# Performance work log

Hardware: AMD Instinct MI355X
Metric: run time of the kernel (lower is better)

The kernel has to match this reference:

```python
import jax, jax.numpy as jnp
import numpy as np

# SOM hyperparameters (match init_kwargs)
M, N_GRID = 32, 32
D = 512
BATCH = 8192
ALPHA = 0.5          # learning_rate
NUM_EPOCH_BP = 5     # hard-coded in call(): self.backprop(self.count, 5)
ITER = 0             # first call: count == 0
RADIUS_FACTOR = 1.1
GAUSSIAN_STD = 0.08
SIGMA = max(M, N_GRID) * RADIUS_FACTOR  # 35.2


def setup_inputs() -> dict:
    key = jax.random.key(0)
    k1, k2 = jax.random.split(key)
    x = jax.random.normal(k1, (BATCH, D), dtype=jnp.float32)
    som_map = jax.random.uniform(k2, (M * N_GRID, D), dtype=jnp.float32)  # RandomUniform(0,1)
    ii, jj = np.meshgrid(np.arange(M), np.arange(N_GRID), indexing='ij')
    locs = jnp.asarray(np.stack([ii.ravel(), jj.ravel()], axis=1), dtype=jnp.int32)  # [N,2]
    return {"x": x, "som_map": som_map, "locs": locs}


def reference(x, som_map, locs):
    # --- feedforward: BMU search ---
    # squared_distance[b,n] = ||x[b] - map[n]||^2, computed without the [B,N,D] blowup
    x2 = jnp.sum(x * x, axis=1, keepdims=True)                 # [B,1]
    m2 = jnp.sum(som_map * som_map, axis=1)[None, :]           # [1,N]
    sqd = x2 + m2 - 2.0 * (x @ som_map.T)                      # [B,N]
    bmu_indices = jnp.argmin(sqd, axis=1)                      # [B]
    bmu_locs = locs[bmu_indices]                               # [B,2] int

    # --- backprop (iter=0, num_epoch=5) ---
    decay = ITER * (ALPHA - 1.0) / (NUM_EPOCH_BP - 1.0)
    radius = SIGMA - decay
    alpha = ALPHA - decay

    # bmu_distance_squares[b,n] = ||locs[n] - bmu_locs[b]||^2 (grid coords)
    diff = locs[None, :, :] - bmu_locs[:, None, :]             # [B,N,2] small (int)
    bmu_d2 = jnp.sum(diff * diff, axis=2).astype(jnp.float32)  # [B,N]
    impact = jnp.exp(-bmu_d2 / (2.0 * (radius * GAUSSIAN_STD) ** 2))  # [B,N]
    lr = impact * alpha                                        # [B,N]

    # weight_update[n,d] = sum_b lr[b,n] * (x[b,d] - map[n,d])
    # = einsum('bn,bd->nd') - map * sum_b lr   (avoids the [B,N,D] intermediate)
    weight_update = jnp.einsum('bn,bd->nd', lr, x) - som_map * jnp.sum(lr, axis=0)[:, None]
    return som_map + weight_update
```

## Files before the change

### kernel.cpp

```cpp
#include <hip/hip_runtime.h>
#include <stdint.h>

#define D 512
#define KTOT 512
#define BATCH 8192
#define NMAP 1024
#define GRID_W 32
#define ALPHA 0.5f
#define C2 15.859712f

typedef __attribute__((ext_vector_type(4))) float f32x4;
typedef __attribute__((ext_vector_type(8))) _Float16 f16x8;
typedef __attribute__((ext_vector_type(8))) unsigned short u16x8;

static __device__ __forceinline__ unsigned short f2h(float f) {
    union { _Float16 h; unsigned short u; } cv;
    cv.h = (_Float16)f;
    return cv.u;
}

__global__ __launch_bounds__(256) void k_prep(const float* __restrict__ x,
                                              const float* __restrict__ map,
                                              unsigned short* __restrict__ As,
                                              unsigned short* __restrict__ Bs,
                                              float* __restrict__ m2,
                                              unsigned long long* __restrict__ packed) {
    int bid = blockIdx.x;
    if (bid < BATCH * (D / 8) / 256) {
        int g = bid * 256 + threadIdx.x;
        if (g < BATCH) packed[g] = 0xFFFFFFFFFFFFFFFFull;
        int b = g >> 6;
        int k8 = (g & 63) << 3;
        const float* xp = x + (size_t)b * D + k8;
        float4 v0 = *(const float4*)xp;
        float4 v1 = *(const float4*)(xp + 4);
        float vv[8] = {v0.x, v0.y, v0.z, v0.w, v1.x, v1.y, v1.z, v1.w};
        u16x8 hi;
        #pragma unroll
        for (int j = 0; j < 8; j++) hi[j] = f2h(vv[j]);
        *(u16x8*)(As + (size_t)b * KTOT + k8) = hi;
    } else {
        int mb = bid - BATCH * (D / 8) / 256;
        int n = mb * 4 + (threadIdx.x >> 6);
        int lane = threadIdx.x & 63;
        const float* mp = map + (size_t)n * D + lane * 8;
        float4 v0 = *(const float4*)mp;
        float4 v1 = *(const float4*)(mp + 4);
        float vv[8] = {v0.x, v0.y, v0.z, v0.w, v1.x, v1.y, v1.z, v1.w};
        u16x8 hi;
        float s = 0.f;
        #pragma unroll
        for (int j = 0; j < 8; j++) {
            s += vv[j] * vv[j];
            hi[j] = f2h(vv[j]);
        }
        *(u16x8*)(Bs + (size_t)n * KTOT + lane * 8) = hi;
        #pragma unroll
        for (int off = 32; off > 0; off >>= 1) s += __shfl_down(s, off);
        if (lane == 0) m2[n] = s;
    }
}

#define BM 128
#define BN 64
#define BK 64

__global__ __launch_bounds__(256) void k_bmu(const unsigned short* __restrict__ As,
                                             const unsigned short* __restrict__ Bs,
                                             const float* __restrict__ m2,
                                             unsigned long long* __restrict__ packed) {
    __shared__ unsigned short Al[BM * BK];
    __shared__ unsigned short Bl[BN * BK];
    const int xcd = blockIdx.x & 7;
    const int j = blockIdx.x >> 3;
    const int b0 = (xcd * 8 + (j & 7)) * BM;
    const int n0 = (j >> 3) * BN;
    const int t = threadIdx.x;
    const int w = t >> 6, l = t & 63;
    const int wm = w >> 1, wn = w & 1;

    f32x4 acc[4][2];
    #pragma unroll
    for (int i = 0; i < 4; i++)
        #pragma unroll
        for (int jj = 0; jj < 2; jj++) acc[i][jj] = (f32x4)(0.f);

    const int srow = l >> 3;
    const int sslot = (l & 7) ^ (l >> 3);
    const unsigned short* agp0 = As + (size_t)(b0 + w * 32 + srow) * KTOT + sslot * 8;
    const unsigned short* bgp0 = Bs + (size_t)(n0 + w * 16 + srow) * KTOT + sslot * 8;

    for (int kt = 0; kt < KTOT; kt += BK) {
        #pragma unroll
        for (int i = 0; i < 4; i++) {
            __builtin_amdgcn_global_load_lds(
                (const __attribute__((address_space(1))) void*)(agp0 + (size_t)i * 8 * KTOT + kt),
                (__attribute__((address_space(3))) void*)(Al + w * 2048 + i * 512), 16, 0, 0);
        }
        #pragma unroll
        for (int i = 0; i < 2; i++) {
            __builtin_amdgcn_global_load_lds(
                (const __attribute__((address_space(1))) void*)(bgp0 + (size_t)i * 8 * KTOT + kt),
                (__attribute__((address_space(3))) void*)(Bl + w * 1024 + i * 512), 16, 0, 0);
        }
        __syncthreads();

        #pragma unroll
        for (int kk = 0; kk < 2; kk++) {
            f16x8 af[4], bfr[2];
            #pragma unroll
            for (int mi = 0; mi < 4; mi++) {
                int r = wm * 64 + mi * 16 + (l & 15);
                int slot = kk * 4 + (l >> 4);
                af[mi] = *(const f16x8*)&Al[r * 64 + ((slot ^ (r & 7)) << 3)];
            }
            #pragma unroll
            for (int nj = 0; nj < 2; nj++) {
                int r = wn * 32 + nj * 16 + (l & 15);
                int slot = kk * 4 + (l >> 4);
                bfr[nj] = *(const f16x8*)&Bl[r * 64 + ((slot ^ (r & 7)) << 3)];
            }
            #pragma unroll
            for (int mi = 0; mi < 4; mi++)
                #pragma unroll
                for (int nj = 0; nj < 2; nj++)
                    acc[mi][nj] = __builtin_amdgcn_mfma_f32_16x16x32_f16(
                        af[mi], bfr[nj], acc[mi][nj], 0, 0, 0);
        }
        __syncthreads();
    }

    float m2v[2];
    #pragma unroll
    for (int nj = 0; nj < 2; nj++)
        m2v[nj] = m2[n0 + wn * 32 + nj * 16 + (l & 15)];

    #pragma unroll
    for (int mi = 0; mi < 4; mi++) {
        #pragma unroll
        for (int reg = 0; reg < 4; reg++) {
            float best = m2v[0] - 2.0f * acc[mi][0][reg];
            int bi = n0 + wn * 32 + (l & 15);
            {
                float v = m2v[1] - 2.0f * acc[mi][1][reg];
                int n = n0 + wn * 32 + 16 + (l & 15);
                if (v < best) { best = v; bi = n; }
            }
            #pragma unroll
            for (int msk = 1; msk <= 8; msk <<= 1) {
                float ov = __shfl_xor(best, msk);
                int oi = __shfl_xor(bi, msk);
                if (ov < best || (ov == best && oi < bi)) { best = ov; bi = oi; }
            }
            if ((l & 15) == 0) {
                unsigned int fb = __float_as_uint(best);
                fb = (fb & 0x80000000u) ? ~fb : (fb | 0x80000000u);
                unsigned long long key =
                    ((unsigned long long)fb << 32) | (unsigned int)bi;
                int row = b0 + wm * 64 + mi * 16 + (l >> 4) * 4 + reg;
                atomicMin(&packed[row], key);
            }
        }
    }
}

__global__ __launch_bounds__(256) void k_scatter(const float* __restrict__ x,
                                                 const unsigned long long* __restrict__ packed,
                                                 float* __restrict__ S,
                                                 int* __restrict__ cnt) {
    __shared__ int list[BATCH];
    __shared__ int cnts[256];
    __shared__ int offs[256];
    int g = blockIdx.x;
    int t = threadIdx.x;
    int b0 = t * (BATCH / 256);

    int mybmu[BATCH / 256];
    int c = 0;
    #pragma unroll
    for (int i = 0; i < BATCH / 256; i++) {
        mybmu[i] = (int)(packed[b0 + i] & 0xFFFFFFFFull);
        c += (mybmu[i] == g) ? 1 : 0;
    }
    cnts[t] = c;
    offs[t] = c;
    __syncthreads();
    #pragma unroll
    for (int s = 1; s < 256; s <<= 1) {
        int v = (t >= s) ? offs[t - s] : 0;
        __syncthreads();
        offs[t] += v;
        __syncthreads();
    }
    int off = offs[t] - cnts[t];
    #pragma unroll
    for (int i = 0; i < BATCH / 256; i++) {
        if (mybmu[i] == g) list[off++] = b0 + i;
    }
    __syncthreads();
    int len = offs[255];

    float a0 = 0.f, a1 = 0.f, c0 = 0.f, c1 = 0.f;
    int i = 0;
    for (; i + 2 <= len; i += 2) {
        const float* xr0 = x + (size_t)list[i] * D;
        const float* xr1 = x + (size_t)list[i + 1] * D;
        a0 += xr0[t]; a1 += xr0[t + 256];
        c0 += xr1[t]; c1 += xr1[t + 256];
    }
    if (i < len) {
        const float* xr = x + (size_t)list[i] * D;
        a0 += xr[t]; a1 += xr[t + 256];
    }
    S[(size_t)g * D + t] = a0 + c0;
    S[(size_t)g * D + t + 256] = a1 + c1;
    if (t == 0) cnt[g] = len;
}

__global__ __launch_bounds__(256) void k_conv1(const float* __restrict__ S,
                                               float* __restrict__ V,
                                               const int* __restrict__ cnt,
                                               float* __restrict__ sum_lr) {
    __shared__ float tbl[GRID_W];
    __shared__ float vc[GRID_W][GRID_W];
    int gi = blockIdx.x;
    int d = blockIdx.y * 256 + threadIdx.x;
    if (threadIdx.x < GRID_W)
        tbl[threadIdx.x] = __expf(-(float)(threadIdx.x * threadIdx.x) / C2);
    __syncthreads();
    float acc[GRID_W];
    #pragma unroll
    for (int nj = 0; nj < GRID_W; nj++) acc[nj] = 0.f;
    for (int gj = 0; gj < GRID_W; gj++) {
        float s = S[(size_t)(gi * GRID_W + gj) * D + d];
        #pragma unroll
        for (int nj = 0; nj < GRID_W; nj++) {
            int dd = nj - gj; dd = dd < 0 ? -dd : dd;
            acc[nj] += tbl[dd] * s;
        }
    }
    #pragma unroll
    for (int nj = 0; nj < GRID_W; nj++)
        V[(size_t)(gi * GRID_W + nj) * D + d] = acc[nj];

    if (blockIdx.x == 0 && blockIdx.y == 0) {
        int t = threadIdx.x;
        #pragma unroll
        for (int j = 0; j < 4; j++) {
            int idx = t * 4 + j;
            int a = idx >> 5, b = idx & 31;
            float s = 0.f;
            for (int gj = 0; gj < GRID_W; gj++) {
                int dd = gj - b; dd = dd < 0 ? -dd : dd;
                s += tbl[dd] * (float)cnt[a * GRID_W + gj];
            }
            vc[a][b] = s;
        }
        __syncthreads();
        #pragma unroll
        for (int j = 0; j < 4; j++) {
            int idx = t * 4 + j;
            int a = idx >> 5, b = idx & 31;
            float s2 = 0.f;
            for (int gg = 0; gg < GRID_W; gg++) {
                int dd = gg - a; dd = dd < 0 ? -dd : dd;
                s2 += tbl[dd] * vc[gg][b];
            }
            sum_lr[idx] = ALPHA * s2;
        }
    }
}

__global__ __launch_bounds__(256) void k_conv2(const float* __restrict__ V,
                                               const float* __restrict__ map,
                                               const float* __restrict__ sum_lr,
                                               float* __restrict__ out) {
    __shared__ float tbl[GRID_W];
    int nj = blockIdx.x;
    int d = blockIdx.y * 256 + threadIdx.x;
    if (threadIdx.x < GRID_W)
        tbl[threadIdx.x] = __expf(-(float)(threadIdx.x * threadIdx.x) / C2);
    __syncthreads();
    float acc[GRID_W];
    #pragma unroll
    for (int ni = 0; ni < GRID_W; ni++) acc[ni] = 0.f;
    for (int gi = 0; gi < GRID_W; gi++) {
        float v = V[(size_t)(gi * GRID_W + nj) * D + d];
        #pragma unroll
        for (int ni = 0; ni < GRID_W; ni++) {
            int dd = ni - gi; dd = dd < 0 ? -dd : dd;
            acc[ni] += tbl[dd] * v;
        }
    }
    #pragma unroll
    for (int ni = 0; ni < GRID_W; ni++) {
        int n = ni * GRID_W + nj;
        out[(size_t)n * D + d] =
            map[(size_t)n * D + d] * (1.0f - sum_lr[n]) + ALPHA * acc[ni];
    }
}

extern "C" void kernel_launch(void* const* d_in, const int* in_sizes, int n_in,
                              void* d_out, int out_size, void* d_ws, size_t ws_size,
                              hipStream_t stream) {
    (void)in_sizes; (void)n_in; (void)out_size; (void)ws_size;
    const float* x = (const float*)d_in[0];
    const float* map = (const float*)d_in[1];
    float* out = (float*)d_out;

    char* ws = (char*)d_ws;
    unsigned long long* packed = (unsigned long long*)(ws);
    float* m2 = (float*)(ws + 65536);
    int* cnt = (int*)(ws + 69632);
    float* sum_lr = (float*)(ws + 73728);
    float* S = (float*)(ws + 77824);
    float* V = (float*)(ws + 2174976);
    unsigned short* As = (unsigned short*)(ws + 4272128);
    unsigned short* Bs = (unsigned short*)(ws + 12660736);

    k_prep<<<BATCH * (D / 8) / 256 + NMAP / 4, 256, 0, stream>>>(x, map, As, Bs, m2, packed);
    k_bmu<<<(BATCH / BM) * (NMAP / BN), 256, 0, stream>>>(As, Bs, m2, packed);
    k_scatter<<<NMAP, 256, 0, stream>>>(x, packed, S, cnt);
    k_conv1<<<dim3(GRID_W, D / 256), 256, 0, stream>>>(S, V, cnt, sum_lr);
    k_conv2<<<dim3(GRID_W, D / 256), 256, 0, stream>>>(V, map, sum_lr, out);
}
```

Before: 83.38 us.

## Double-buffer LDS tiles in BMU GEMM to overlap global loads with MFMA

The BMU distance GEMM now keeps two LDS buffers for the A and B tiles. The next K-tile is issued with global_load_lds while MFMAs run on the current tile, and one barrier per iteration is dropped. The aim is to hide global-to-LDS latency behind compute. In exchange, LDS use doubles (to 48KB per block), which may lower occupancy. The barrier at the end of the loop has to cover completion of the asynchronous loads.

```diff
diff --git a/kernel.cpp b/kernel.cpp
--- a/kernel.cpp
+++ b/kernel.cpp
@@ -69,8 +69,8 @@
                                              const unsigned short* __restrict__ Bs,
                                              const float* __restrict__ m2,
                                              unsigned long long* __restrict__ packed) {
-    __shared__ unsigned short Al[BM * BK];
-    __shared__ unsigned short Bl[BN * BK];
+    __shared__ unsigned short Al[2][BM * BK];
+    __shared__ unsigned short Bl[2][BN * BK];
     const int xcd = blockIdx.x & 7;
     const int j = blockIdx.x >> 3;
     const int b0 = (xcd * 8 + (j & 7)) * BM;
@@ -90,21 +90,27 @@
     const unsigned short* agp0 = As + (size_t)(b0 + w * 32 + srow) * KTOT + sslot * 8;
     const unsigned short* bgp0 = Bs + (size_t)(n0 + w * 16 + srow) * KTOT + sslot * 8;
 
-    for (int kt = 0; kt < KTOT; kt += BK) {
-        #pragma unroll
-        for (int i = 0; i < 4; i++) {
-            __builtin_amdgcn_global_load_lds(
-                (const __attribute__((address_space(1))) void*)(agp0 + (size_t)i * 8 * KTOT + kt),
-                (__attribute__((address_space(3))) void*)(Al + w * 2048 + i * 512), 16, 0, 0);
-        }
-        #pragma unroll
-        for (int i = 0; i < 2; i++) {
-            __builtin_amdgcn_global_load_lds(
-                (const __attribute__((address_space(1))) void*)(bgp0 + (size_t)i * 8 * KTOT + kt),
-                (__attribute__((address_space(3))) void*)(Bl + w * 1024 + i * 512), 16, 0, 0);
-        }
-        __syncthreads();
-
+    #define STAGE(BUF, KT)                                                        \
+    do {                                                                          \
+        _Pragma("unroll")                                                         \
+        for (int i = 0; i < 4; i++) {                                             \
+            __builtin_amdgcn_global_load_lds(                                     \
+                (const __attribute__((address_space(1))) void*)(agp0 + (size_t)i * 8 * KTOT + (KT)), \
+                (__attribute__((address_space(3))) void*)(&Al[BUF][w * 2048 + i * 512]), 16, 0, 0); \
+        }                                                                         \
+        _Pragma("unroll")                                                         \
+        for (int i = 0; i < 2; i++) {                                             \
+            __builtin_amdgcn_global_load_lds(                                     \
+                (const __attribute__((address_space(1))) void*)(bgp0 + (size_t)i * 8 * KTOT + (KT)), \
+                (__attribute__((address_space(3))) void*)(&Bl[BUF][w * 1024 + i * 512]), 16, 0, 0); \
+        }                                                                         \
+    } while (0)
+
+    STAGE(0, 0);
+    __syncthreads();
+    int cur = 0;
+    for (int tt = 0; tt < KTOT / BK; ++tt) {
+        if (tt < KTOT / BK - 1) STAGE(cur ^ 1, (tt + 1) * BK);
         #pragma unroll
         for (int kk = 0; kk < 2; kk++) {
             f16x8 af[4], bfr[2];
@@ -112,13 +118,13 @@
             for (int mi = 0; mi < 4; mi++) {
                 int r = wm * 64 + mi * 16 + (l & 15);
                 int slot = kk * 4 + (l >> 4);
-                af[mi] = *(const f16x8*)&Al[r * 64 + ((slot ^ (r & 7)) << 3)];
+                af[mi] = *(const f16x8*)&Al[cur][r * 64 + ((slot ^ (r & 7)) << 3)];
             }
             #pragma unroll
             for (int nj = 0; nj < 2; nj++) {
                 int r = wn * 32 + nj * 16 + (l & 15);
                 int slot = kk * 4 + (l >> 4);
-                bfr[nj] = *(const f16x8*)&Bl[r * 64 + ((slot ^ (r & 7)) << 3)];
+                bfr[nj] = *(const f16x8*)&Bl[cur][r * 64 + ((slot ^ (r & 7)) << 3)];
             }
             #pragma unroll
             for (int mi = 0; mi < 4; mi++)
@@ -128,7 +134,9 @@
                         af[mi], bfr[nj], acc[mi][nj], 0, 0, 0);
         }
         __syncthreads();
-    }
+        cur ^= 1;
+    }
+    #undef STAGE
 
     float m2v[2];
     #pragma unroll
```

Measured after the change: 94.11 us. 12.9% more time.
